# Optimization experiments

Measured on AMD Instinct MI355X. Metric: run time of the kernel, lower is better.

## Reference

```python
import jax, jax.numpy as jnp
import numpy as np
import math

IN_DIM = 256
OUT_DIM = 256
MAX_IN = 1024
MAX_OUT = 512
BATCH = 2
SEQ = 1024  # actual_seq_len == max_in_seq here
RED = 2
LN_EPS = 1e-5


def setup_inputs() -> dict:
    key = jax.random.key(0)
    ks = jax.random.split(key, 8)
    N = BATCH * SEQ
    return {
        "x": jax.random.normal(ks[0], (N, IN_DIM), dtype=jnp.float32),
        "M": jax.random.uniform(ks[1], (OUT_DIM, IN_DIM), minval=-0.5, maxval=0.5, dtype=jnp.float32),
        "P": jax.random.uniform(ks[2], (OUT_DIM, OUT_DIM), minval=-0.1, maxval=0.1, dtype=jnp.float32),
        "Linker": jax.random.uniform(ks[3], (MAX_IN, MAX_OUT), minval=-0.1, maxval=0.1, dtype=jnp.float32),
        "ln_gamma": jnp.ones((OUT_DIM,), dtype=jnp.float32),
        "ln_beta": jnp.zeros((OUT_DIM,), dtype=jnp.float32),
        "res_W": jax.random.uniform(ks[4], (OUT_DIM, IN_DIM), minval=-0.1, maxval=0.1, dtype=jnp.float32),
        "res_linker": jax.random.uniform(ks[5], (MAX_IN, MAX_OUT), minval=-0.1, maxval=0.1, dtype=jnp.float32),
        "actual_seq_len": SEQ,
    }


def _layer_norm(z, gamma, beta):
    mu = jnp.mean(z, axis=-1, keepdims=True)
    var = jnp.mean((z - mu) ** 2, axis=-1, keepdims=True)
    return (z - mu) * jax.lax.rsqrt(var + LN_EPS) * gamma + beta


def _periods():
    i = jnp.arange(OUT_DIM, dtype=jnp.float32)[:, None]
    j = jnp.arange(OUT_DIM, dtype=jnp.float32)[None, :]
    return i * OUT_DIM + j + 2.0  # (D, D)


def reference(x, M, P, Linker, ln_gamma, ln_beta, res_W, res_linker, actual_seq_len):
    S = int(actual_seq_len)
    N, _ = x.shape
    B = N // S
    D = OUT_DIM
    out_seq = max(1, S // RED)

    # Z = LN(x @ M^T)
    Z = _layer_norm(x @ M.T, ln_gamma, ln_beta)  # (N, D)

    # position transform: T[k,i] = sum_j Z[k,j] * P[i,j] * cos(2*pi*k / periods[i,j])
    k = jnp.arange(N, dtype=jnp.float32)[:, None, None]  # (N,1,1)
    phi = jnp.cos(2.0 * math.pi * k / _periods()[None])   # (N, D, D)
    T = jnp.einsum('kj,ij,kij->ki', Z, P, phi)            # (N, D)

    # adaptive sequence-length transform via Linker slice
    L = Linker[:S, :out_seq]                               # (S, out_seq)
    U = jnp.einsum('bsd,st->btd', T.reshape(B, S, D), L).reshape(B * out_seq, D)

    # 'separate' residual path
    rfeat = (x @ res_W.T).reshape(B, S, D)
    rL = res_linker[:S, :out_seq]
    residual = jnp.einsum('bsd,st->btd', rfeat, rL).reshape(B * out_seq, D)

    return U + residual
```

## Files before the change

kernel.cpp:

```cpp
#include <hip/hip_runtime.h>

#define D256 256
#define S_SEQ 1024
#define OUTSEQ 512

typedef __attribute__((ext_vector_type(8))) short bf16x8;
typedef __attribute__((ext_vector_type(8))) unsigned short u16x8;
typedef __attribute__((ext_vector_type(4))) unsigned short u16x4;
typedef __attribute__((ext_vector_type(4))) float f32x4;
typedef __attribute__((ext_vector_type(2))) float f32x2;

__device__ inline unsigned short f2bf(float f) {
  unsigned u = __float_as_uint(f);
  return (unsigned short)((u + 0x7fffu + ((u >> 16) & 1u)) >> 16);
}

__device__ inline bf16x8 ld8bf(const float* p) {
  const float4 v0 = *(const float4*)p;
  const float4 v1 = *(const float4*)(p + 4);
  bf16x8 r;
  r[0] = (short)f2bf(v0.x); r[1] = (short)f2bf(v0.y);
  r[2] = (short)f2bf(v0.z); r[3] = (short)f2bf(v0.w);
  r[4] = (short)f2bf(v1.x); r[5] = (short)f2bf(v1.y);
  r[6] = (short)f2bf(v1.z); r[7] = (short)f2bf(v1.w);
  return r;
}

__global__ __launch_bounds__(256) void k_pre(const float* __restrict__ x,
                                             const float* __restrict__ M,
                                             const float* __restrict__ resW,
                                             const float* __restrict__ P,
                                             const float* __restrict__ Linker,
                                             const float* __restrict__ rLinker,
                                             const float* __restrict__ gamma,
                                             const float* __restrict__ beta,
                                             float4* __restrict__ PIt4,
                                             unsigned short* __restrict__ LinkTb,
                                             float* __restrict__ Zb,
                                             unsigned short* __restrict__ Bt) {
  __shared__ float smem[8224];
  const int tid = threadIdx.x;
  const int blk = blockIdx.x;

  if (blk < 128) {
    float (*Zs)[D256] = (float(*)[D256])smem;
    float (*Rs)[D256] = (float(*)[D256])(smem + 4096);
    float* mu_s = smem + 8192;
    float* rs_s = smem + 8208;
    const int k0 = blk * 16;
    const int w = tid >> 6;
    const int l = tid & 63;
    const int m = l & 15, q = l >> 4;

    f32x4 aZ[4] = {}, aR[4] = {};
    const float* xrow = x + (size_t)(k0 + m) * D256;
    #pragma unroll
    for (int ks = 0; ks < 8; ++ks) {
      const bf16x8 a = ld8bf(xrow + ks * 32 + q * 8);
      #pragma unroll
      for (int cf = 0; cf < 4; ++cf) {
        const int o = w * 64 + cf * 16 + m;
        const bf16x8 bz = ld8bf(M    + (size_t)o * D256 + ks * 32 + q * 8);
        const bf16x8 br = ld8bf(resW + (size_t)o * D256 + ks * 32 + q * 8);
        aZ[cf] = __builtin_amdgcn_mfma_f32_16x16x32_bf16(a, bz, aZ[cf], 0, 0, 0);
        aR[cf] = __builtin_amdgcn_mfma_f32_16x16x32_bf16(a, br, aR[cf], 0, 0, 0);
      }
    }
    #pragma unroll
    for (int cf = 0; cf < 4; ++cf) {
      #pragma unroll
      for (int r = 0; r < 4; ++r) {
        Zs[q * 4 + r][w * 64 + cf * 16 + m] = aZ[cf][r];
        Rs[q * 4 + r][w * 64 + cf * 16 + m] = aR[cf][r];
      }
    }
    __syncthreads();

    #pragma unroll
    for (int rr = w; rr < 16; rr += 4) {
      float s = 0.f, sq = 0.f;
      #pragma unroll
      for (int p = 0; p < 4; ++p) {
        const float v = Zs[rr][l + 64 * p];
        s += v;
        sq = fmaf(v, v, sq);
      }
      #pragma unroll
      for (int off = 32; off; off >>= 1) {
        s += __shfl_down(s, off);
        sq += __shfl_down(sq, off);
      }
      if (l == 0) {
        const float mu = s * (1.0f / 256.0f);
        const float var = sq * (1.0f / 256.0f) - mu * mu;
        mu_s[rr] = mu;
        rs_s[rr] = rsqrtf(var + 1e-5f);
      }
    }
    __syncthreads();

    {
      const int t = tid;
      const float g = gamma[t], be = beta[t];
      u16x8 o0, o1;
      #pragma unroll
      for (int rr = 0; rr < 16; ++rr) {
        Zb[(size_t)(k0 + rr) * D256 + t] = (Zs[rr][t] - mu_s[rr]) * rs_s[rr] * g + be;
        const unsigned short rb = f2bf(Rs[rr][t]);
        if (rr < 8) o0[rr] = rb; else o1[rr - 8] = rb;
      }
      unsigned short* dst = Bt + (size_t)t * 4096 + 2048 + k0;
      *(u16x8*)dst = o0;
      *(u16x8*)(dst + 8) = o1;
    }
    return;
  }

  if (blk < 384) {
    const int j = blk - 128;
    const int t = tid;
    const float p = (float)(t * D256 + j + 2);
    const float ip = 1.0f / p;
    const float cb2 = 2.0f * __builtin_amdgcn_cosf(ip);
    const float D = fmaf(cb2, cb2, -2.0f);
    PIt4[j * D256 + t] = make_float4(P[t * D256 + j], ip, cb2, D);
    return;
  }

  float (*tl)[65] = (float(*)[65])smem;
  const int tb = blk - 384;
  const int st = tb & 31;
  const int tt = tb >> 5;
  const int s0 = st * 64, t0 = tt * 64;
  const float* src = (s0 < 1024) ? (Linker + (size_t)s0 * OUTSEQ)
                                 : (rLinker + (size_t)(s0 - 1024) * OUTSEQ);
  {
    const int sy = tid >> 2, sx = tid & 3;
    #pragma unroll
    for (int c = 0; c < 4; ++c) {
      const int ci = sx + c * 4;
      const float4 v = *(const float4*)&src[sy * OUTSEQ + t0 + ci * 4];
      tl[ci * 4 + 0][sy] = v.x;
      tl[ci * 4 + 1][sy] = v.y;
      tl[ci * 4 + 2][sy] = v.z;
      tl[ci * 4 + 3][sy] = v.w;
    }
  }
  __syncthreads();
  {
    const int ty = tid >> 2, tx = tid & 3;
    u16x8 o0, o1;
    #pragma unroll
    for (int e = 0; e < 8; ++e) o0[e] = f2bf(tl[ty][tx * 16 + e]);
    #pragma unroll
    for (int e = 0; e < 8; ++e) o1[e] = f2bf(tl[ty][tx * 16 + 8 + e]);
    unsigned short* dst = LinkTb + (size_t)(t0 + ty) * 2048 + s0 + tx * 16;
    *(u16x8*)dst = o0;
    *(u16x8*)(dst + 8) = o1;
  }
}

__global__ __launch_bounds__(256, 6) void k_B(const float* __restrict__ Zb,
                                              const float4* __restrict__ PIt4,
                                              unsigned short* __restrict__ Bt) {
  __shared__ float buf[5120];
  const int tid = threadIdx.x;
  const int il = tid & 7;
  const int jg = tid >> 3;
  const int ig = blockIdx.x & 31;
  const int kt = blockIdx.x >> 5;
  const int i0 = ig * 8;
  const int k0 = kt * 16;
  const int i  = i0 + il;

  #pragma unroll
  for (int r = 0; r < 16; ++r)
    buf[tid * 20 + r] = Zb[(size_t)(k0 + r) * D256 + tid];
  __syncthreads();

  f32x2 acc[8];
  #pragma unroll
  for (int q = 0; q < 8; ++q) acc[q] = (f32x2){0.f, 0.f};

  const float kf0 = (float)k0;
  const f32x4* pip = (const f32x4*)(PIt4 + i);
  #pragma unroll
  for (int jj = 0; jj < 8; ++jj) {
    const int j = jg + 32 * jj;
    const f32x4 pi = pip[(size_t)j * D256];
    const float4 z0 = *(const float4*)&buf[j * 20 + 0];
    const float4 z1 = *(const float4*)&buf[j * 20 + 4];
    const float4 z2 = *(const float4*)&buf[j * 20 + 8];
    const float4 z3 = *(const float4*)&buf[j * 20 + 12];
    const float a  = kf0 * pi.y;
    const float r0 = __builtin_amdgcn_fractf(a);
    const float r1 = __builtin_amdgcn_fractf(a + pi.y);
    const float s0 = __builtin_amdgcn_cosf(r0) * pi.x;
    const float s1 = __builtin_amdgcn_cosf(r1) * pi.x;
    const float s2 = fmaf(pi.z, s1, -s0);
    const float s3 = fmaf(pi.z, s2, -s1);
    f32x2 P0 = {s0, s1};
    f32x2 P1 = {s2, s3};
    const f32x2 D2 = {pi.w, pi.w};
    acc[0] = __builtin_elementwise_fma((f32x2){z0.x, z0.y}, P0, acc[0]);
    acc[1] = __builtin_elementwise_fma((f32x2){z0.z, z0.w}, P1, acc[1]);
    f32x2 Pn;
#define CSTEP(IDX, ZA, ZB) \
    Pn = __builtin_elementwise_fma(D2, P1, -P0); \
    acc[IDX] = __builtin_elementwise_fma((f32x2){ZA, ZB}, Pn, acc[IDX]); \
    P0 = P1; P1 = Pn;
    CSTEP(2, z1.x, z1.y)
    CSTEP(3, z1.z, z1.w)
    CSTEP(4, z2.x, z2.y)
    CSTEP(5, z2.z, z2.w)
    CSTEP(6, z3.x, z3.y)
    CSTEP(7, z3.z, z3.w)
#undef CSTEP
  }
  __syncthreads();

  #pragma unroll
  for (int k2 = 0; k2 < 8; ++k2) {
    buf[jg * 132 + (k2 * 2) * 8 + il]     = acc[k2].x;
    buf[jg * 132 + (k2 * 2 + 1) * 8 + il] = acc[k2].y;
  }
  __syncthreads();

  float tv = 0.f;
  if (tid < 128) {
    #pragma unroll
    for (int g = 0; g < 32; ++g) tv += buf[g * 132 + tid];
  }
  __syncthreads();
  if (tid < 128) buf[(tid & 7) * 16 + (tid >> 3)] = tv;
  __syncthreads();
  if (tid < 32) {
    const int iw = tid >> 2;
    const int kq = tid & 3;
    const float4 v = *(const float4*)&buf[iw * 16 + kq * 4];
    u16x4 o;
    o[0] = f2bf(v.x); o[1] = f2bf(v.y); o[2] = f2bf(v.z); o[3] = f2bf(v.w);
    *(u16x4*)(Bt + (size_t)(i0 + iw) * 4096 + k0 + kq * 4) = o;
  }
}

__global__ __launch_bounds__(256) void k_Cm(const unsigned short* __restrict__ LinkTb,
                                            const unsigned short* __restrict__ Bt,
                                            float* __restrict__ out) {
  __shared__ float red[4][16][32];
  const int bid = blockIdx.x;
  const int ct = bid & 7;
  const int tt = (bid >> 3) & 31;
  const int b  = bid >> 8;
  const int t0 = tt * 16;
  const int d0 = ct * 32;
  const int w  = threadIdx.x >> 6;
  const int l  = threadIdx.x & 63;
  const int m  = l & 15, q = l >> 4;
  const int seg = w >> 1;
  const int sh  = w & 1;

  f32x4 acc0 = {}, acc1 = {};
  const unsigned short* Arow = LinkTb + (size_t)(t0 + m) * 2048 + seg * 1024 + sh * 512 + q * 8;
  const unsigned short* Brow = Bt + (size_t)(d0 + m) * 4096 + seg * 2048 + b * 1024 + sh * 512 + q * 8;

  #pragma unroll
  for (int ks = 0; ks < 16; ++ks) {
    const bf16x8 a0 = *(const bf16x8*)(Arow + ks * 32);
    const bf16x8 b0 = *(const bf16x8*)(Brow + ks * 32);
    const bf16x8 b1 = *(const bf16x8*)(Brow + 16 * 4096 + ks * 32);
    acc0 = __builtin_amdgcn_mfma_f32_16x16x32_bf16(a0, b0, acc0, 0, 0, 0);
    acc1 = __builtin_amdgcn_mfma_f32_16x16x32_bf16(a0, b1, acc1, 0, 0, 0);
  }

  #pragma unroll
  for (int r = 0; r < 4; ++r) {
    red[w][q * 4 + r][m]      = acc0[r];
    red[w][q * 4 + r][16 + m] = acc1[r];
  }
  __syncthreads();

  const int row = threadIdx.x >> 4;
  const int c0  = (threadIdx.x & 15) * 2;
  float2 s;
  s.x = red[0][row][c0] + red[1][row][c0] + red[2][row][c0] + red[3][row][c0];
  s.y = red[0][row][c0 + 1] + red[1][row][c0 + 1] + red[2][row][c0 + 1] + red[3][row][c0 + 1];
  *(float2*)&out[(size_t)(b * 512 + t0 + row) * D256 + d0 + c0] = s;
}

extern "C" void kernel_launch(void* const* d_in, const int* in_sizes, int n_in,
                              void* d_out, int out_size, void* d_ws, size_t ws_size,
                              hipStream_t stream) {
  const float* x       = (const float*)d_in[0];
  const float* M       = (const float*)d_in[1];
  const float* P       = (const float*)d_in[2];
  const float* Linker  = (const float*)d_in[3];
  const float* gamma   = (const float*)d_in[4];
  const float* beta    = (const float*)d_in[5];
  const float* resW    = (const float*)d_in[6];
  const float* rLinker = (const float*)d_in[7];
  float* out = (float*)d_out;

  char* ws = (char*)d_ws;
  float4*         PIt4   = (float4*)(ws);
  unsigned short* LinkTb = (unsigned short*)(ws + 1024 * 1024);
  unsigned short* Bt     = (unsigned short*)(ws + 3072 * 1024);
  float*          Zb     = (float*)(ws + 5120 * 1024);

  hipLaunchKernelGGL(k_pre, dim3(640),  dim3(256), 0, stream,
                     x, M, resW, P, Linker, rLinker, gamma, beta,
                     PIt4, LinkTb, Zb, Bt);
  hipLaunchKernelGGL(k_B,   dim3(4096), dim3(256), 0, stream, Zb, PIt4, Bt);
  hipLaunchKernelGGL(k_Cm,  dim3(512),  dim3(256), 0, stream, LinkTb, Bt, out);
}
```

Baseline: 54.45 us.

## Fuse all stages into one cooperative persistent kernel with grid syncs

Merges the prep, projection+LayerNorm, position-transform and final GEMM stages into one cooperative kernel of 1024 blocks separated by grid.sync, with a multi-kernel fallback when occupancy is insufficient. Inputs x, M and resW are now pre-converted to bf16 in a separate prep phase, and the B phase processes four i-groups per block so it fits the persistent grid. The aim is to remove kernel launch gaps and tail effects. In exchange it adds grid-wide barriers, leaves many blocks idle in the projection phase, lowers occupancy to 4 blocks per CU, and calls an occupancy query on every launch.

```diff
diff --git a/kernel.cpp b/kernel.cpp
--- a/kernel.cpp
+++ b/kernel.cpp
@@ -1,4 +1,7 @@
 #include <hip/hip_runtime.h>
+#include <hip/hip_cooperative_groups.h>
+
+namespace cg = cooperative_groups;
 
 #define D256 256
 #define S_SEQ 1024
@@ -15,109 +18,16 @@
   return (unsigned short)((u + 0x7fffu + ((u >> 16) & 1u)) >> 16);
 }
 
-__device__ inline bf16x8 ld8bf(const float* p) {
-  const float4 v0 = *(const float4*)p;
-  const float4 v1 = *(const float4*)(p + 4);
-  bf16x8 r;
-  r[0] = (short)f2bf(v0.x); r[1] = (short)f2bf(v0.y);
-  r[2] = (short)f2bf(v0.z); r[3] = (short)f2bf(v0.w);
-  r[4] = (short)f2bf(v1.x); r[5] = (short)f2bf(v1.y);
-  r[6] = (short)f2bf(v1.z); r[7] = (short)f2bf(v1.w);
-  return r;
-}
-
-__global__ __launch_bounds__(256) void k_pre(const float* __restrict__ x,
-                                             const float* __restrict__ M,
-                                             const float* __restrict__ resW,
-                                             const float* __restrict__ P,
-                                             const float* __restrict__ Linker,
-                                             const float* __restrict__ rLinker,
-                                             const float* __restrict__ gamma,
-                                             const float* __restrict__ beta,
-                                             float4* __restrict__ PIt4,
-                                             unsigned short* __restrict__ LinkTb,
-                                             float* __restrict__ Zb,
-                                             unsigned short* __restrict__ Bt) {
-  __shared__ float smem[8224];
-  const int tid = threadIdx.x;
-  const int blk = blockIdx.x;
-
-  if (blk < 128) {
-    float (*Zs)[D256] = (float(*)[D256])smem;
-    float (*Rs)[D256] = (float(*)[D256])(smem + 4096);
-    float* mu_s = smem + 8192;
-    float* rs_s = smem + 8208;
-    const int k0 = blk * 16;
-    const int w = tid >> 6;
-    const int l = tid & 63;
-    const int m = l & 15, q = l >> 4;
-
-    f32x4 aZ[4] = {}, aR[4] = {};
-    const float* xrow = x + (size_t)(k0 + m) * D256;
-    #pragma unroll
-    for (int ks = 0; ks < 8; ++ks) {
-      const bf16x8 a = ld8bf(xrow + ks * 32 + q * 8);
-      #pragma unroll
-      for (int cf = 0; cf < 4; ++cf) {
-        const int o = w * 64 + cf * 16 + m;
-        const bf16x8 bz = ld8bf(M    + (size_t)o * D256 + ks * 32 + q * 8);
-        const bf16x8 br = ld8bf(resW + (size_t)o * D256 + ks * 32 + q * 8);
-        aZ[cf] = __builtin_amdgcn_mfma_f32_16x16x32_bf16(a, bz, aZ[cf], 0, 0, 0);
-        aR[cf] = __builtin_amdgcn_mfma_f32_16x16x32_bf16(a, br, aR[cf], 0, 0, 0);
-      }
-    }
-    #pragma unroll
-    for (int cf = 0; cf < 4; ++cf) {
-      #pragma unroll
-      for (int r = 0; r < 4; ++r) {
-        Zs[q * 4 + r][w * 64 + cf * 16 + m] = aZ[cf][r];
-        Rs[q * 4 + r][w * 64 + cf * 16 + m] = aR[cf][r];
-      }
-    }
-    __syncthreads();
-
-    #pragma unroll
-    for (int rr = w; rr < 16; rr += 4) {
-      float s = 0.f, sq = 0.f;
-      #pragma unroll
-      for (int p = 0; p < 4; ++p) {
-        const float v = Zs[rr][l + 64 * p];
-        s += v;
-        sq = fmaf(v, v, sq);
-      }
-      #pragma unroll
-      for (int off = 32; off; off >>= 1) {
-        s += __shfl_down(s, off);
-        sq += __shfl_down(sq, off);
-      }
-      if (l == 0) {
-        const float mu = s * (1.0f / 256.0f);
-        const float var = sq * (1.0f / 256.0f) - mu * mu;
-        mu_s[rr] = mu;
-        rs_s[rr] = rsqrtf(var + 1e-5f);
-      }
-    }
-    __syncthreads();
-
-    {
-      const int t = tid;
-      const float g = gamma[t], be = beta[t];
-      u16x8 o0, o1;
-      #pragma unroll
-      for (int rr = 0; rr < 16; ++rr) {
-        Zb[(size_t)(k0 + rr) * D256 + t] = (Zs[rr][t] - mu_s[rr]) * rs_s[rr] * g + be;
-        const unsigned short rb = f2bf(Rs[rr][t]);
-        if (rr < 8) o0[rr] = rb; else o1[rr - 8] = rb;
-      }
-      unsigned short* dst = Bt + (size_t)t * 4096 + 2048 + k0;
-      *(u16x8*)dst = o0;
-      *(u16x8*)(dst + 8) = o1;
-    }
-    return;
-  }
-
-  if (blk < 384) {
-    const int j = blk - 128;
+
+__device__ __forceinline__ void phase_prep(int blk, int tid, float* smem,
+                                           const float* x, const float* M,
+                                           const float* resW, const float* P,
+                                           const float* Linker, const float* rLinker,
+                                           float4* PIt4, unsigned short* LinkTb,
+                                           unsigned short* xb, unsigned short* Mb,
+                                           unsigned short* Wb) {
+  if (blk < 256) {
+    const int j = blk;
     const int t = tid;
     const float p = (float)(t * D256 + j + 2);
     const float ip = 1.0f / p;
@@ -126,9 +36,24 @@
     PIt4[j * D256 + t] = make_float4(P[t * D256 + j], ip, cb2, D);
     return;
   }
-
+  if (blk >= 512) {
+    const float* src;
+    unsigned short* dst;
+    size_t base;
+    if (blk < 768)      { src = x;    dst = xb; base = (size_t)(blk - 512) * 2048; }
+    else if (blk < 800) { src = M;    dst = Mb; base = (size_t)(blk - 768) * 2048; }
+    else                { src = resW; dst = Wb; base = (size_t)(blk - 800) * 2048; }
+    const size_t off = base + (size_t)tid * 8;
+    const float4 v0 = *(const float4*)(src + off);
+    const float4 v1 = *(const float4*)(src + off + 4);
+    u16x8 o;
+    o[0] = f2bf(v0.x); o[1] = f2bf(v0.y); o[2] = f2bf(v0.z); o[3] = f2bf(v0.w);
+    o[4] = f2bf(v1.x); o[5] = f2bf(v1.y); o[6] = f2bf(v1.z); o[7] = f2bf(v1.w);
+    *(u16x8*)(dst + off) = o;
+    return;
+  }
   float (*tl)[65] = (float(*)[65])smem;
-  const int tb = blk - 384;
+  const int tb = blk - 256;
   const int st = tb & 31;
   const int tt = tb >> 5;
   const int s0 = st * 64, t0 = tt * 64;
@@ -160,102 +85,185 @@
   }
 }
 
-__global__ __launch_bounds__(256, 6) void k_B(const float* __restrict__ Zb,
-                                              const float4* __restrict__ PIt4,
-                                              unsigned short* __restrict__ Bt) {
-  __shared__ float buf[5120];
-  const int tid = threadIdx.x;
+__device__ __forceinline__ void phase_azn(int blk, int tid, float* smem,
+                                          const unsigned short* xb,
+                                          const unsigned short* Mb,
+                                          const unsigned short* Wb,
+                                          const float* gamma, const float* beta,
+                                          float* Zb, unsigned short* Bt) {
+  float (*Zs)[D256] = (float(*)[D256])smem;
+  float (*Rs)[D256] = (float(*)[D256])(smem + 4096);
+  float* mu_s = smem + 8192;
+  float* rs_s = smem + 8208;
+  const int k0 = blk * 16;
+  const int w = tid >> 6;
+  const int l = tid & 63;
+  const int m = l & 15, q = l >> 4;
+
+  f32x4 aZ[4] = {}, aR[4] = {};
+  const unsigned short* Arow = xb + (size_t)(k0 + m) * D256;
+  #pragma unroll
+  for (int ks = 0; ks < 8; ++ks) {
+    const bf16x8 a = *(const bf16x8*)(Arow + ks * 32 + q * 8);
+    #pragma unroll
+    for (int cf = 0; cf < 4; ++cf) {
+      const int o = w * 64 + cf * 16 + m;
+      const bf16x8 bz = *(const bf16x8*)(Mb + (size_t)o * D256 + ks * 32 + q * 8);
+      const bf16x8 br = *(const bf16x8*)(Wb + (size_t)o * D256 + ks * 32 + q * 8);
+      aZ[cf] = __builtin_amdgcn_mfma_f32_16x16x32_bf16(a, bz, aZ[cf], 0, 0, 0);
+      aR[cf] = __builtin_amdgcn_mfma_f32_16x16x32_bf16(a, br, aR[cf], 0, 0, 0);
+    }
+  }
+  #pragma unroll
+  for (int cf = 0; cf < 4; ++cf) {
+    #pragma unroll
+    for (int r = 0; r < 4; ++r) {
+      Zs[q * 4 + r][w * 64 + cf * 16 + m] = aZ[cf][r];
+      Rs[q * 4 + r][w * 64 + cf * 16 + m] = aR[cf][r];
+    }
+  }
+  __syncthreads();
+
+  #pragma unroll
+  for (int rr = w; rr < 16; rr += 4) {
+    float s = 0.f, sq = 0.f;
+    #pragma unroll
+    for (int p = 0; p < 4; ++p) {
+      const float v = Zs[rr][l + 64 * p];
+      s += v;
+      sq = fmaf(v, v, sq);
+    }
+    #pragma unroll
+    for (int off = 32; off; off >>= 1) {
+      s += __shfl_down(s, off);
+      sq += __shfl_down(sq, off);
+    }
+    if (l == 0) {
+      const float mu = s * (1.0f / 256.0f);
+      const float var = sq * (1.0f / 256.0f) - mu * mu;
+      mu_s[rr] = mu;
+      rs_s[rr] = rsqrtf(var + 1e-5f);
+    }
+  }
+  __syncthreads();
+
+  {
+    const int t = tid;
+    const float g = gamma[t], be = beta[t];
+    u16x8 o0, o1;
+    #pragma unroll
+    for (int rr = 0; rr < 16; ++rr) {
+      Zb[(size_t)(k0 + rr) * D256 + t] = (Zs[rr][t] - mu_s[rr]) * rs_s[rr] * g + be;
+      const unsigned short rb = f2bf(Rs[rr][t]);
+      if (rr < 8) o0[rr] = rb; else o1[rr - 8] = rb;
+    }
+    unsigned short* dst = Bt + (size_t)t * 4096 + 2048 + k0;
+    *(u16x8*)dst = o0;
+    *(u16x8*)(dst + 8) = o1;
+  }
+}
+
+__device__ __forceinline__ void phase_b(int bid, int tid, float* smem,
+                                        const float* Zb, const float4* PIt4,
+                                        unsigned short* Bt) {
+  float* buf  = smem;
+  float* rbuf = smem + 5120;
   const int il = tid & 7;
   const int jg = tid >> 3;
-  const int ig = blockIdx.x & 31;
-  const int kt = blockIdx.x >> 5;
-  const int i0 = ig * 8;
+  const int kt = bid >> 3;
+  const int ig0 = (bid & 7) * 4;
   const int k0 = kt * 16;
-  const int i  = i0 + il;
 
   #pragma unroll
   for (int r = 0; r < 16; ++r)
     buf[tid * 20 + r] = Zb[(size_t)(k0 + r) * D256 + tid];
   __syncthreads();
 
-  f32x2 acc[8];
-  #pragma unroll
-  for (int q = 0; q < 8; ++q) acc[q] = (f32x2){0.f, 0.f};
-
   const float kf0 = (float)k0;
-  const f32x4* pip = (const f32x4*)(PIt4 + i);
-  #pragma unroll
-  for (int jj = 0; jj < 8; ++jj) {
-    const int j = jg + 32 * jj;
-    const f32x4 pi = pip[(size_t)j * D256];
-    const float4 z0 = *(const float4*)&buf[j * 20 + 0];
-    const float4 z1 = *(const float4*)&buf[j * 20 + 4];
-    const float4 z2 = *(const float4*)&buf[j * 20 + 8];
-    const float4 z3 = *(const float4*)&buf[j * 20 + 12];
-    const float a  = kf0 * pi.y;
-    const float r0 = __builtin_amdgcn_fractf(a);
-    const float r1 = __builtin_amdgcn_fractf(a + pi.y);
-    const float s0 = __builtin_amdgcn_cosf(r0) * pi.x;
-    const float s1 = __builtin_amdgcn_cosf(r1) * pi.x;
-    const float s2 = fmaf(pi.z, s1, -s0);
-    const float s3 = fmaf(pi.z, s2, -s1);
-    f32x2 P0 = {s0, s1};
-    f32x2 P1 = {s2, s3};
-    const f32x2 D2 = {pi.w, pi.w};
-    acc[0] = __builtin_elementwise_fma((f32x2){z0.x, z0.y}, P0, acc[0]);
-    acc[1] = __builtin_elementwise_fma((f32x2){z0.z, z0.w}, P1, acc[1]);
-    f32x2 Pn;
+  #pragma unroll 1
+  for (int v = 0; v < 4; ++v) {
+    const int ig = ig0 + v;
+    const int i0 = ig * 8;
+    const int i  = i0 + il;
+
+    f32x2 acc[8];
+    #pragma unroll
+    for (int q = 0; q < 8; ++q) acc[q] = (f32x2){0.f, 0.f};
+
+    const f32x4* pip = (const f32x4*)(PIt4 + i);
+    #pragma unroll
+    for (int jj = 0; jj < 8; ++jj) {
+      const int j = jg + 32 * jj;
+      const f32x4 pi = pip[(size_t)j * D256];
+      const float4 z0 = *(const float4*)&buf[j * 20 + 0];
+      const float4 z1 = *(const float4*)&buf[j * 20 + 4];
+      const float4 z2 = *(const float4*)&buf[j * 20 + 8];
+      const float4 z3 = *(const float4*)&buf[j * 20 + 12];
+      const float a  = kf0 * pi.y;
+      const float r0 = __builtin_amdgcn_fractf(a);
+      const float r1 = __builtin_amdgcn_fractf(a + pi.y);
+      const float s0 = __builtin_amdgcn_cosf(r0) * pi.x;
+      const float s1 = __builtin_amdgcn_cosf(r1) * pi.x;
+      const float s2 = fmaf(pi.z, s1, -s0);
+      const float s3 = fmaf(pi.z, s2, -s1);
+      f32x2 P0 = {s0, s1};
+      f32x2 P1 = {s2, s3};
+      const f32x2 D2 = {pi.w, pi.w};
+      acc[0] = __builtin_elementwise_fma((f32x2){z0.x, z0.y}, P0, acc[0]);
+      acc[1] = __builtin_elementwise_fma((f32x2){z0.z, z0.w}, P1, acc[1]);
+      f32x2 Pn;
 #define CSTEP(IDX, ZA, ZB) \
-    Pn = __builtin_elementwise_fma(D2, P1, -P0); \
-    acc[IDX] = __builtin_elementwise_fma((f32x2){ZA, ZB}, Pn, acc[IDX]); \
-    P0 = P1; P1 = Pn;
-    CSTEP(2, z1.x, z1.y)
-    CSTEP(3, z1.z, z1.w)
-    CSTEP(4, z2.x, z2.y)
-    CSTEP(5, z2.z, z2.w)
-    CSTEP(6, z3.x, z3.y)
-    CSTEP(7, z3.z, z3.w)
+      Pn = __builtin_elementwise_fma(D2, P1, -P0); \
+      acc[IDX] = __builtin_elementwise_fma((f32x2){ZA, ZB}, Pn, acc[IDX]); \
+      P0 = P1; P1 = Pn;
+      CSTEP(2, z1.x, z1.y)
+      CSTEP(3, z1.z, z1.w)
+      CSTEP(4, z2.x, z2.y)
+      CSTEP(5, z2.z, z2.w)
+      CSTEP(6, z3.x, z3.y)
+      CSTEP(7, z3.z, z3.w)
 #undef CSTEP
-  }
-  __syncthreads();
-
-  #pragma unroll
-  for (int k2 = 0; k2 < 8; ++k2) {
-    buf[jg * 132 + (k2 * 2) * 8 + il]     = acc[k2].x;
-    buf[jg * 132 + (k2 * 2 + 1) * 8 + il] = acc[k2].y;
-  }
-  __syncthreads();
-
-  float tv = 0.f;
-  if (tid < 128) {
-    #pragma unroll
-    for (int g = 0; g < 32; ++g) tv += buf[g * 132 + tid];
-  }
-  __syncthreads();
-  if (tid < 128) buf[(tid & 7) * 16 + (tid >> 3)] = tv;
-  __syncthreads();
-  if (tid < 32) {
-    const int iw = tid >> 2;
-    const int kq = tid & 3;
-    const float4 v = *(const float4*)&buf[iw * 16 + kq * 4];
-    u16x4 o;
-    o[0] = f2bf(v.x); o[1] = f2bf(v.y); o[2] = f2bf(v.z); o[3] = f2bf(v.w);
-    *(u16x4*)(Bt + (size_t)(i0 + iw) * 4096 + k0 + kq * 4) = o;
-  }
-}
-
-__global__ __launch_bounds__(256) void k_Cm(const unsigned short* __restrict__ LinkTb,
-                                            const unsigned short* __restrict__ Bt,
-                                            float* __restrict__ out) {
-  __shared__ float red[4][16][32];
-  const int bid = blockIdx.x;
+    }
+
+    #pragma unroll
+    for (int k2 = 0; k2 < 8; ++k2) {
+      rbuf[jg * 132 + (k2 * 2) * 8 + il]     = acc[k2].x;
+      rbuf[jg * 132 + (k2 * 2 + 1) * 8 + il] = acc[k2].y;
+    }
+    __syncthreads();
+
+    float tv = 0.f;
+    if (tid < 128) {
+      #pragma unroll
+      for (int g = 0; g < 32; ++g) tv += rbuf[g * 132 + tid];
+    }
+    __syncthreads();
+    if (tid < 128) rbuf[(tid & 7) * 16 + (tid >> 3)] = tv;
+    __syncthreads();
+    if (tid < 32) {
+      const int iw = tid >> 2;
+      const int kq = tid & 3;
+      const float4 vv = *(const float4*)&rbuf[iw * 16 + kq * 4];
+      u16x4 o;
+      o[0] = f2bf(vv.x); o[1] = f2bf(vv.y); o[2] = f2bf(vv.z); o[3] = f2bf(vv.w);
+      *(u16x4*)(Bt + (size_t)(i0 + iw) * 4096 + k0 + kq * 4) = o;
+    }
+    __syncthreads();
+  }
+}
+
+__device__ __forceinline__ void phase_cm(int bid, int tid, float* smem,
+                                         const unsigned short* LinkTb,
+                                         const unsigned short* Bt,
+                                         float* out) {
+#define RED(w, r, c) smem[(((w) * 16 + (r)) * 32) + (c)]
   const int ct = bid & 7;
   const int tt = (bid >> 3) & 31;
   const int b  = bid >> 8;
   const int t0 = tt * 16;
   const int d0 = ct * 32;
-  const int w  = threadIdx.x >> 6;
-  const int l  = threadIdx.x & 63;
+  const int w  = tid >> 6;
+  const int l  = tid & 63;
   const int m  = l & 15, q = l >> 4;
   const int seg = w >> 1;
   const int sh  = w & 1;
@@ -275,17 +283,79 @@
 
   #pragma unroll
   for (int r = 0; r < 4; ++r) {
-    red[w][q * 4 + r][m]      = acc0[r];
-    red[w][q * 4 + r][16 + m] = acc1[r];
+    RED(w, q * 4 + r, m)      = acc0[r];
+    RED(w, q * 4 + r, 16 + m) = acc1[r];
   }
   __syncthreads();
 
-  const int row = threadIdx.x >> 4;
-  const int c0  = (threadIdx.x & 15) * 2;
+  const int row = tid >> 4;
+  const int c0  = (tid & 15) * 2;
   float2 s;
-  s.x = red[0][row][c0] + red[1][row][c0] + red[2][row][c0] + red[3][row][c0];
-  s.y = red[0][row][c0 + 1] + red[1][row][c0 + 1] + red[2][row][c0 + 1] + red[3][row][c0 + 1];
+  s.x = RED(0, row, c0) + RED(1, row, c0) + RED(2, row, c0) + RED(3, row, c0);
+  s.y = RED(0, row, c0 + 1) + RED(1, row, c0 + 1) + RED(2, row, c0 + 1) + RED(3, row, c0 + 1);
   *(float2*)&out[(size_t)(b * 512 + t0 + row) * D256 + d0 + c0] = s;
+#undef RED
+}
+
+__global__ __launch_bounds__(256, 4) void k_all(const float* x, const float* M,
+                                                const float* resW, const float* P,
+                                                const float* Linker, const float* rLinker,
+                                                const float* gamma, const float* beta,
+                                                float4* PIt4, unsigned short* LinkTb,
+                                                unsigned short* xb, unsigned short* Mb,
+                                                unsigned short* Wb, float* Zb,
+                                                unsigned short* Bt, float* out) {
+  __shared__ float smem[9344];
+  cg::grid_group grid = cg::this_grid();
+  const int tid = threadIdx.x;
+  const int bid = blockIdx.x;
+
+  if (bid < 832)
+    phase_prep(bid, tid, smem, x, M, resW, P, Linker, rLinker,
+               PIt4, LinkTb, xb, Mb, Wb);
+  grid.sync();
+
+  if (bid < 128)
+    phase_azn(bid, tid, smem, xb, Mb, Wb, gamma, beta, Zb, Bt);
+  grid.sync();
+
+  phase_b(bid, tid, smem, Zb, PIt4, Bt);
+  grid.sync();
+
+  if (bid < 512)
+    phase_cm(bid, tid, smem, LinkTb, Bt, out);
+}
+
+__global__ __launch_bounds__(256) void k_s_pre(const float* x, const float* M,
+                                               const float* resW, const float* P,
+                                               const float* Linker, const float* rLinker,
+                                               float4* PIt4, unsigned short* LinkTb,
+                                               unsigned short* xb, unsigned short* Mb,
+                                               unsigned short* Wb) {
+  __shared__ float smem[4160];
+  phase_prep(blockIdx.x, threadIdx.x, smem, x, M, resW, P, Linker, rLinker,
+             PIt4, LinkTb, xb, Mb, Wb);
+}
+
+__global__ __launch_bounds__(256) void k_s_azn(const unsigned short* xb,
+                                               const unsigned short* Mb,
+                                               const unsigned short* Wb,
+                                               const float* gamma, const float* beta,
+                                               float* Zb, unsigned short* Bt) {
+  __shared__ float smem[8224];
+  phase_azn(blockIdx.x, threadIdx.x, smem, xb, Mb, Wb, gamma, beta, Zb, Bt);
+}
+
+__global__ __launch_bounds__(256, 4) void k_s_b(const float* Zb, const float4* PIt4,
+                                                unsigned short* Bt) {
+  __shared__ float smem[9344];
+  phase_b(blockIdx.x, threadIdx.x, smem, Zb, PIt4, Bt);
+}
+
+__global__ __launch_bounds__(256) void k_s_cm(const unsigned short* LinkTb,
+                                              const unsigned short* Bt, float* out) {
+  __shared__ float smem[2048];
+  phase_cm(blockIdx.x, threadIdx.x, smem, LinkTb, Bt, out);
 }
 
 extern "C" void kernel_launch(void* const* d_in, const int* in_sizes, int n_in,
@@ -305,11 +375,26 @@
   float4*         PIt4   = (float4*)(ws);
   unsigned short* LinkTb = (unsigned short*)(ws + 1024 * 1024);
   unsigned short* Bt     = (unsigned short*)(ws + 3072 * 1024);
-  float*          Zb     = (float*)(ws + 5120 * 1024);
-
-  hipLaunchKernelGGL(k_pre, dim3(640),  dim3(256), 0, stream,
-                     x, M, resW, P, Linker, rLinker, gamma, beta,
-                     PIt4, LinkTb, Zb, Bt);
-  hipLaunchKernelGGL(k_B,   dim3(4096), dim3(256), 0, stream, Zb, PIt4, Bt);
-  hipLaunchKernelGGL(k_Cm,  dim3(512),  dim3(256), 0, stream, LinkTb, Bt, out);
-}
+  unsigned short* xb     = (unsigned short*)(ws + 5120 * 1024);
+  unsigned short* Mb     = (unsigned short*)(ws + 6144 * 1024);
+  unsigned short* Wb     = (unsigned short*)(ws + 6272 * 1024);
+  float*          Zb     = (float*)(ws + 6400 * 1024);
+
+  int nb = 0;
+  (void)hipOccupancyMaxActiveBlocksPerMultiprocessor(&nb, k_all, 256, 0);
+
+  if (nb >= 4) {
+    void* args[] = {(void*)&x, (void*)&M, (void*)&resW, (void*)&P,
+                    (void*)&Linker, (void*)&rLinker, (void*)&gamma, (void*)&beta,
+                    (void*)&PIt4, (void*)&LinkTb, (void*)&xb, (void*)&Mb,
+                    (void*)&Wb, (void*)&Zb, (void*)&Bt, (void*)&out};
+    hipLaunchCooperativeKernel(k_all, dim3(1024), dim3(256), args, 0, stream);
+  } else {
+    hipLaunchKernelGGL(k_s_pre, dim3(832),  dim3(256), 0, stream,
+                       x, M, resW, P, Linker, rLinker, PIt4, LinkTb, xb, Mb, Wb);
+    hipLaunchKernelGGL(k_s_azn, dim3(128),  dim3(256), 0, stream,
+                       xb, Mb, Wb, gamma, beta, Zb, Bt);
+    hipLaunchKernelGGL(k_s_b,   dim3(1024), dim3(256), 0, stream, Zb, PIt4, Bt);
+    hipLaunchKernelGGL(k_s_cm,  dim3(512),  dim3(256), 0, stream, LinkTb, Bt, out);
+  }
+}
```

Result: faster. 51.08 us (-6.2%).
